# Optimization experiments

Measured on AMD Instinct MI355X. Metric: run time of the kernel, lower is better.

Reference implementation:

```python
import jax, jax.numpy as jnp
import numpy as np


def setup_inputs() -> dict:
    key = jax.random.key(0)
    k0, k1, k2, k3 = jax.random.split(key, 4)
    B, S, D, F, E = 8, 2048, 1024, 2048, 8
    x = jax.random.normal(k0, (B, S, D), dtype=jnp.float32)
    Wg = jax.random.normal(k1, (D, E), dtype=jnp.float32) * 0.02
    W1 = jax.random.normal(k2, (E, D, F), dtype=jnp.float32) * 0.02
    W2 = jax.random.normal(k3, (E, F, D), dtype=jnp.float32) * 0.02
    return {"x": x, "Wg": Wg, "W1": W1, "W2": W2}


def reference(x, Wg, W1, W2):
    # Expert-choice MoE: experts pick top-C tokens, conflicts resolved by
    # max router prob (ties -> lowest expert index, matching the serial loop).
    B, S, D = x.shape
    E = Wg.shape[1]
    T = B * S
    cap = max(1, T // E)  # capacity_factor = 1.0

    xt = x.reshape(T, D)
    logits = xt @ Wg                      # [T, E]
    probs = jax.nn.softmax(logits, axis=-1)
    pT = probs.T                          # [E, T] token affinities per expert

    _, top_idx = jax.lax.top_k(pT, cap)   # [E, cap] tokens chosen by each expert
    sel = jnp.zeros((E, T), dtype=bool).at[jnp.arange(E)[:, None], top_idx].set(True)

    # Serial conflict loop is equivalent to: per token, pick the selecting
    masked = jnp.where(sel, pT, -jnp.inf)
    assigned = sel.any(axis=0)            # [T]
    tok2exp = jnp.where(assigned,
                        jnp.argmax(masked, axis=0),
                        jnp.argmax(pT, axis=0))          # [T] int
    weights = jnp.take_along_axis(probs, tok2exp[:, None], axis=1)[:, 0]  # [T]

    # Dispatch / expert FFN / weighted combine. Loop over the small fixed
    # expert set; masked tokens contribute exactly zero, matching index_add_.
    out = jnp.zeros_like(xt)
    for e in range(E):
        gate = jnp.where(tok2exp == e, weights, 0.0)     # [T]
        h = jax.nn.gelu(xt @ W1[e], approximate=False) @ W2[e]  # [T, D]
        out = out + gate[:, None] * h

    return out.reshape(B, S, D)
```

## Files before the change

kernel.cpp:

```cpp
#include <hip/hip_runtime.h>
#include <hip/hip_bf16.h>
#include <math.h>

#define T_TOK 16384
#define DIM   1024
#define FF    2048
#define NE    8
#define CAPK  2048
#define WL1SZ 4096
#define WL2SZ 2048

typedef unsigned short u16;
typedef unsigned long long u64;
typedef __attribute__((ext_vector_type(8))) short bf16x8;
typedef __attribute__((ext_vector_type(4))) float f32x4;

__device__ __forceinline__ u16 f2bf(float f) {
  __hip_bfloat16 h = __float2bfloat16(f);
  union { __hip_bfloat16 h; u16 u; } c; c.h = h; return c.u;
}

__device__ __forceinline__ float gelu_f(float v) {
  float z = fabsf(v) * 0.70710678118654752f;
  float t = __builtin_amdgcn_rcpf(1.0f + 0.3275911f * z);
  float poly = t * (0.254829592f +
               t * (-0.284496736f +
               t * (1.421413741f +
               t * (-1.453152027f +
               t * 1.061405429f))));
  float ez = __expf(-z * z);
  float erfz = 1.0f - poly * ez;
  erfz = copysignf(erfz, v);
  return 0.5f * v * (1.0f + erfz);
}

__device__ __forceinline__ void async_copy16(const void* g, void* l) {
  __builtin_amdgcn_global_load_lds(
      (const __attribute__((address_space(1))) unsigned int*)g,
      (__attribute__((address_space(3))) unsigned int*)l, 16, 0, 0);
}

__device__ __forceinline__ bf16x8 ds_read16(const char* p) {
  bf16x8 r;
  asm volatile("ds_read_b128 %0, %1"
               : "=&v"(r)
               : "v"((const __attribute__((address_space(3))) char*)p));
  return r;
}

#define LGKM0()                                                                   \
  do {                                                                            \
    asm volatile("s_waitcnt lgkmcnt(0)" ::: "memory");                            \
    __builtin_amdgcn_sched_barrier(0);                                            \
  } while (0)
#define VMW0() asm volatile("s_waitcnt vmcnt(0)" ::: "memory")
#define BAR() asm volatile("s_barrier" ::: "memory")

__global__ __launch_bounds__(256) void prep_k(const float* __restrict__ x,
                                              const float* __restrict__ Wg,
                                              const float* __restrict__ W1,
                                              const float* __restrict__ W2,
                                              float* __restrict__ probs,
                                              float* __restrict__ probsT,
                                              u16* __restrict__ xb,
                                              u16* __restrict__ w1t,
                                              u16* __restrict__ w2t,
                                              u64* __restrict__ key,
                                              int* cnt, int* cnt2, int* gates) {
  __shared__ float tile[64][65];
  int bid = blockIdx.x, tid = threadIdx.x;
  if (bid < 4096) {
    if (tid < 4) key[bid * 4 + tid] = 0ull;
    if (bid == 0 && tid < NE) { cnt[tid] = 0; cnt2[tid] = 0; }
    if (bid == 0 && tid >= 8 && tid < 10) gates[tid - 8] = 0;
    int wid = tid >> 6, lane = tid & 63;
    int t = bid * 4 + wid;
    const float* xr = x + (size_t)t * DIM;
    u16* xbr = xb + (size_t)t * DIM;
    double acc[NE] = {0, 0, 0, 0, 0, 0, 0, 0};
#pragma unroll 1
    for (int it = 0; it < DIM / 64; ++it) {
      int d = it * 64 + lane;
      float xv = xr[d];
      xbr[d] = f2bf(xv);
      const float4* wrow = (const float4*)(Wg + (size_t)d * NE);
      float4 w0 = wrow[0], w1 = wrow[1];
      acc[0] += (double)xv * (double)w0.x;
      acc[1] += (double)xv * (double)w0.y;
      acc[2] += (double)xv * (double)w0.z;
      acc[3] += (double)xv * (double)w0.w;
      acc[4] += (double)xv * (double)w1.x;
      acc[5] += (double)xv * (double)w1.y;
      acc[6] += (double)xv * (double)w1.z;
      acc[7] += (double)xv * (double)w1.w;
    }
#pragma unroll
    for (int e = 0; e < NE; ++e)
      for (int o = 32; o > 0; o >>= 1) acc[e] += __shfl_down(acc[e], o, 64);
    if (lane == 0) {
      float l[NE], mx = -3.0e38f;
#pragma unroll
      for (int e = 0; e < NE; ++e) { l[e] = (float)acc[e]; mx = fmaxf(mx, l[e]); }
      float s = 0.f;
#pragma unroll
      for (int e = 0; e < NE; ++e) { l[e] = expf(l[e] - mx); s += l[e]; }
      float inv = 1.0f / s;
#pragma unroll
      for (int e = 0; e < NE; ++e) {
        float p = l[e] * inv;
        probs[(size_t)t * NE + e] = p;
        probsT[(size_t)e * T_TOK + t] = p;
      }
    }
  } else {
    int tz = bid - 4096;
    int z = tz >> 9, bxy = tz & 511;
    const float* src;
    u16* dst;
    int R, C;
    if (z < 8) { src = W1 + (size_t)z * DIM * FF; dst = w1t + (size_t)z * DIM * FF; R = DIM; C = FF; }
    else       { src = W2 + (size_t)(z - 8) * FF * DIM; dst = w2t + (size_t)(z - 8) * FF * DIM; R = FF; C = DIM; }
    int nbx = C >> 6;
    int bx = bxy % nbx, by = bxy / nbx;
    int r0 = by * 64, c0 = bx * 64;
    int lr = tid >> 4, lc4 = (tid & 15) * 4;
#pragma unroll
    for (int p = 0; p < 4; ++p) {
      float4 v = *(const float4*)(src + (size_t)(r0 + p * 16 + lr) * C + c0 + lc4);
      tile[p * 16 + lr][lc4 + 0] = v.x;
      tile[p * 16 + lr][lc4 + 1] = v.y;
      tile[p * 16 + lr][lc4 + 2] = v.z;
      tile[p * 16 + lr][lc4 + 3] = v.w;
    }
    __syncthreads();
    int oc = tid >> 3, orr = (tid & 7) * 8;
#pragma unroll
    for (int p = 0; p < 2; ++p) {
      int c = p * 32 + oc;
      u16 h[8];
#pragma unroll
      for (int j = 0; j < 8; ++j) h[j] = f2bf(tile[orr + j][c]);
      *(uint4*)(dst + (size_t)(c0 + c) * R + r0 + orr) = *(uint4*)h;
    }
  }
}

__global__ __launch_bounds__(256) void moe_route_k(const float* __restrict__ probsT,
                                                   const float* __restrict__ probs,
                                                   u64* __restrict__ key,
                                                   int* __restrict__ tok2exp,
                                                   float* __restrict__ wgt,
                                                   int* cnt, int* cnt2,
                                                   int* __restrict__ list,
                                                   int* basep, int* wl1, int* wl2,
                                                   int* gates) {
  __shared__ float pcol[T_TOK];
  __shared__ unsigned whist[8][2048];
  __shared__ unsigned hist[2048];
  __shared__ unsigned bcast[2];
  __shared__ unsigned wsum[4];
  __shared__ int wps[4];
  int bid = blockIdx.x, tid = threadIdx.x, wid = tid >> 6, lane = tid & 63;
  if (bid < 8) {
    int e = bid;
    const float4* src4 = (const float4*)(probsT + (size_t)e * T_TOK);
    for (int i = tid; i < T_TOK / 4; i += 256) ((float4*)pcol)[i] = src4[i];
    for (int i = tid; i < 8 * 2048; i += 256) ((unsigned*)whist)[i] = 0;
    unsigned prefix = 0, remaining = CAPK;
#pragma unroll 1
    for (int lvl = 0; lvl < 3; ++lvl) {
      int nb = (lvl == 2) ? 1024 : 2048;
      if (lvl == 0) {
        __syncthreads();
        for (int i = tid; i < T_TOK; i += 256)
          atomicAdd(&whist[wid][__float_as_uint(pcol[i]) >> 21], 1u);
        __syncthreads();
        for (int j = tid; j < 2048; j += 256) {
          unsigned s2 = 0;
#pragma unroll
          for (int w = 0; w < 8; ++w) s2 += whist[w][j];
          hist[j] = s2;
        }
        __syncthreads();
      } else {
        for (int i = tid; i < 2048; i += 256) hist[i] = 0;
        __syncthreads();
        for (int i = tid; i < T_TOK; i += 256) {
          unsigned k = __float_as_uint(pcol[i]);
          bool m = (lvl == 1) ? ((k >> 21) == prefix) : ((k >> 10) == prefix);
          if (m) atomicAdd(&hist[(lvl == 1) ? ((k >> 10) & 2047u) : (k & 1023u)], 1u);
        }
        __syncthreads();
      }
      int nper = nb / 256;
      unsigned cv = 0;
      for (int j = 0; j < nper; ++j) cv += hist[tid * nper + j];
      unsigned s = cv;
#pragma unroll
      for (int o = 1; o < 64; o <<= 1) {
        unsigned tv = __shfl_down(s, o, 64);
        if (lane + o < 64) s += tv;
      }
      if (lane == 0) wsum[wid] = s;
      __syncthreads();
      unsigned above = 0;
      for (int w = wid + 1; w < 4; ++w) above += wsum[w];
      unsigned Sincl = s + above, Sexcl = Sincl - cv;
      if (Sincl >= remaining && Sexcl < remaining) {
        unsigned rem2 = remaining - Sexcl, cum2 = 0;
        for (int j = nper - 1; j >= 0; --j) {
          unsigned h = hist[tid * nper + j];
          if (cum2 + h >= rem2) { bcast[0] = (unsigned)(tid * nper + j); bcast[1] = rem2 - cum2; break; }
          cum2 += h;
        }
      }
      __syncthreads();
      unsigned b = bcast[0];
      remaining = bcast[1];
      prefix = (lvl == 0) ? b : (lvl == 1) ? ((prefix << 11) | b) : ((prefix << 10) | b);
      __syncthreads();
    }
    unsigned vk = prefix;
    int need = (int)remaining;
    const int CH = T_TOK / 256;
    int i0 = tid * CH;
    int myt = 0;
    for (int i = i0; i < i0 + CH; ++i)
      myt += (__float_as_uint(pcol[i]) == vk);
    int p = myt;
#pragma unroll
    for (int o = 1; o < 64; o <<= 1) {
      int tv = __shfl_up(p, o, 64);
      if (lane >= o) p += tv;
    }
    if (lane == 63) wps[wid] = p;
    __syncthreads();
    int wo = 0;
    for (int w = 0; w < wid; ++w) wo += wps[w];
    int run = wo + p - myt;
    u64 ebits = (u64)(7 - e);
    for (int i = i0; i < i0 + CH; ++i) {
      unsigned k = __float_as_uint(pcol[i]);
      bool sv = false;
      if (k > vk) sv = true;
      else if (k == vk) { if (run < need) sv = true; run++; }
      if (sv) atomicMax(&key[i], ((u64)k << 3) | ebits);
    }
    __threadfence();
    __syncthreads();
    if (tid == 0) atomicAdd(&gates[0], 1);
  } else {
    if (tid == 0) {
      while (atomicAdd(&gates[0], 0) < 8) __builtin_amdgcn_s_sleep(8);
    }
    __syncthreads();
    __threadfence();
    int gid = (bid - 8) * 256 + tid;
    u64 k = key[gid];
    int best;
    float bp;
    if (k) {
      best = 7 - (int)(k & 7);
      bp = __uint_as_float((unsigned)(k >> 3));
    } else {
      best = 0; bp = -3.0e38f;
#pragma unroll
      for (int e = 0; e < NE; ++e) {
        float p = probs[(size_t)gid * NE + e];
        if (p > bp) { bp = p; best = e; }
      }
    }
    tok2exp[gid] = best;
    wgt[gid] = bp;
#pragma unroll
    for (int e = 0; e < NE; ++e) {
      u64 m = __ballot(best == e);
      if (best == e && lane == __ffsll(m) - 1) atomicAdd(&cnt[e], (int)__popcll(m));
    }
    __threadfence();
    __syncthreads();
    if (tid == 0) atomicAdd(&gates[1], 1);
    if (tid == 0) {
      while (atomicAdd(&gates[1], 0) < 64) __builtin_amdgcn_s_sleep(8);
    }
    __syncthreads();
    __threadfence();
    int c[NE];
#pragma unroll
    for (int e = 0; e < NE; ++e) c[e] = cnt[e];
    if (gid < NE) {
      int r = 0;
      for (int e = 0; e < gid; ++e) r += c[e];
      basep[gid] = r;
    }
    if (gid < WL1SZ) {
      int e = gid & 7, j = gid >> 3;
      int mte = (c[e] + 127) >> 7;
      wl1[gid] = (j < mte * 16) ? (e | ((j >> 4) << 4) | ((j & 15) << 12)) : -1;
    }
    if (gid >= WL1SZ && gid < WL1SZ + WL2SZ) {
      int g2 = gid - WL1SZ;
      int e = g2 & 7, j = g2 >> 3;
      int mte = (c[e] + 127) >> 7;
      wl2[g2] = (j < mte * 8) ? (e | ((j >> 3) << 4) | ((j & 7) << 12)) : -1;
    }
    int te = tok2exp[gid];
    int bp_e = 0;
#pragma unroll
    for (int e = 0; e < NE; ++e) if (e < te) bp_e += c[e];
    int sl = 0;
#pragma unroll
    for (int e = 0; e < NE; ++e) {
      u64 m = __ballot(te == e);
      if (te == e) {
        int leader = __ffsll(m) - 1;
        int rank = __popcll(m & ((1ull << lane) - 1));
        int b = 0;
        if (lane == leader) b = atomicAdd(&cnt2[e], (int)__popcll(m));
        b = __shfl(b, leader, 64);
        sl = bp_e + b + rank;
      }
    }
    list[sl] = gid;
  }
}


#define MF(M, N_, AV, BV) acc[M][N_] = __builtin_amdgcn_mfma_f32_16x16x32_bf16(BV, AV, acc[M][N_], 0, 0, 0)

#define STG(kt)                                                                   \
  do {                                                                            \
    char* dA = sm;                                                                \
    char* dB = sm + 16384;                                                        \
    size_t ko = (size_t)(kt) * 128;                                               \
    async_copy16(aP0 + ko,      dA + tid * 16);                                   \
    async_copy16(aP1 + ko,      dA + 4096 + tid * 16);                            \
    async_copy16(aP0 + ko + 64, dA + 8192 + tid * 16);                            \
    async_copy16(aP1 + ko + 64, dA + 12288 + tid * 16);                           \
    async_copy16(bP0 + ko,      dB + tid * 16);                                   \
    async_copy16(bP1 + ko,      dB + 4096 + tid * 16);                            \
    async_copy16(bP0 + ko + 64, dB + 8192 + tid * 16);                            \
    async_copy16(bP1 + ko + 64, dB + 12288 + tid * 16);                           \
  } while (0)

#define DSRD(kkoff)                                                               \
  do {                                                                            \
    const char* pa = sm + (kkoff) + wr * 4096 + laneOff;                          \
    const char* pb = sm + 16384 + (kkoff) + wc * 4096 + laneOff;                  \
    a0 = ds_read16(pa);        a1 = ds_read16(pa + 1024);                         \
    a2 = ds_read16(pa + 2048); a3 = ds_read16(pa + 3072);                         \
    b0 = ds_read16(pb);        b1 = ds_read16(pb + 1024);                         \
    b2 = ds_read16(pb + 2048); b3 = ds_read16(pb + 3072);                         \
  } while (0)

#define MFMA16()                                                                  \
  do {                                                                            \
    __builtin_amdgcn_s_setprio(1);                                                \
    MF(0, 0, a0, b0); MF(0, 1, a0, b1); MF(0, 2, a0, b2); MF(0, 3, a0, b3);       \
    MF(1, 0, a1, b0); MF(1, 1, a1, b1); MF(1, 2, a1, b2); MF(1, 3, a1, b3);       \
    MF(2, 0, a2, b0); MF(2, 1, a2, b1); MF(2, 2, a2, b2); MF(2, 3, a2, b3);       \
    MF(3, 0, a3, b0); MF(3, 1, a3, b1); MF(3, 2, a3, b2); MF(3, 3, a3, b3);       \
    __builtin_amdgcn_s_setprio(0);                                                \
  } while (0)

template <int EPI>
__global__ __launch_bounds__(256, 4) void ffn_k(const u16* __restrict__ A,
                                                const u16* __restrict__ Bm,
                                                void* __restrict__ Out,
                                                const int* __restrict__ list,
                                                const float* __restrict__ wgt,
                                                const int* __restrict__ basep,
                                                const int* __restrict__ cnt,
                                                const int* __restrict__ wl) {
  constexpr int K = EPI ? FF : DIM;
  constexpr int N = EPI ? DIM : FF;
  constexpr int KT = K / 64;

  const int wle = wl[blockIdx.x];
  if (wle < 0) return;
  const int e = wle & 15, mt = (wle >> 4) & 255, nt = wle >> 12;
  const int ce = cnt[e];
  const int be = basep[e];

  __shared__ u16 smem[16384];
  __shared__ int toks[128];
  __shared__ float wsc[128];
  char* const sm = (char*)smem;

  const int tid = threadIdx.x;
  if (tid < 128) {
    int r = mt * 128 + tid;
    int tk = (r < ce) ? list[be + r] : list[be];
    toks[tid] = tk;
    if (EPI == 1) wsc[tid] = wgt[tk];
  }
  __syncthreads();

  const int wid = tid >> 6, lane = tid & 63;
  const int wr = wid >> 1, wc = wid & 1;
  (void)wid;
  const int laneOff = ((lane & 15) >> 1) * 128 + (lane & 1) * 64 +
                      (((lane >> 4) << 4) ^ ((((lane & 15) >> 1) & 3) << 4));

  const int r0 = 2 * (tid >> 3) + ((tid & 7) >> 2);
  const int cbl = ((tid & 3) << 4) ^ (((tid >> 3) & 3) << 4);
  const char *aP0, *aP1;
  if (EPI == 0) {
    aP0 = (const char*)(A + (size_t)toks[r0] * K) + cbl;
    aP1 = (const char*)(A + (size_t)toks[r0 + 64] * K) + cbl;
  } else {
    aP0 = (const char*)(A + ((size_t)be + mt * 128 + r0) * K) + cbl;
    aP1 = (const char*)(A + ((size_t)be + mt * 128 + r0 + 64) * K) + cbl;
  }
  const char* bP0 = (const char*)(Bm + ((size_t)e * N + nt * 128 + r0) * K) + cbl;
  const char* bP1 = (const char*)(Bm + ((size_t)e * N + nt * 128 + r0 + 64) * K) + cbl;

  f32x4 acc[4][4];
#pragma unroll
  for (int m = 0; m < 4; ++m)
#pragma unroll
    for (int n = 0; n < 4; ++n) acc[m][n] = (f32x4){0.f, 0.f, 0.f, 0.f};

  bf16x8 a0, a1, a2, a3, b0, b1, b2, b3;

#pragma unroll 1
  for (int kt = 0; kt < KT; ++kt) {
    STG(kt);
    VMW0();
    BAR();
    DSRD(0);
    LGKM0();
    MFMA16();
    DSRD(8192);
    LGKM0();
    MFMA16();
    BAR();
  }

  const int lc = lane & 15, lq = (lane >> 4) * 4;
#pragma unroll
  for (int m = 0; m < 4; ++m) {
    int trow = wr * 64 + m * 16 + lc;
    int grow = mt * 128 + trow;
    if (grow < ce) {
      if (EPI == 0) {
        size_t rowoff = (size_t)(be + grow) * FF + nt * 128 + wc * 64 + lq;
#pragma unroll
        for (int n = 0; n < 4; ++n) {
          ushort4 h4;
          h4.x = f2bf(gelu_f(acc[m][n][0]));
          h4.y = f2bf(gelu_f(acc[m][n][1]));
          h4.z = f2bf(gelu_f(acc[m][n][2]));
          h4.w = f2bf(gelu_f(acc[m][n][3]));
          *(ushort4*)((u16*)Out + rowoff + n * 16) = h4;
        }
      } else {
        float w = wsc[trow];
        size_t rowoff = (size_t)toks[trow] * DIM + nt * 128 + wc * 64 + lq;
#pragma unroll
        for (int n = 0; n < 4; ++n) {
          float4 o = make_float4(w * acc[m][n][0], w * acc[m][n][1],
                                 w * acc[m][n][2], w * acc[m][n][3]);
          *(float4*)((float*)Out + rowoff + n * 16) = o;
        }
      }
    }
  }
}

extern "C" void kernel_launch(void* const* d_in, const int* in_sizes, int n_in,
                              void* d_out, int out_size, void* d_ws, size_t ws_size,
                              hipStream_t stream) {
  (void)in_sizes; (void)n_in; (void)out_size; (void)ws_size;
  const float* x  = (const float*)d_in[0];
  const float* Wg = (const float*)d_in[1];
  const float* W1 = (const float*)d_in[2];
  const float* W2 = (const float*)d_in[3];
  float* out = (float*)d_out;

  char* ws = (char*)d_ws;
  size_t off = 0;
  auto alloc = [&](size_t bytes) -> void* {
    void* p = ws + off;
    off += (bytes + 255) & ~(size_t)255;
    return p;
  };
  u16* xb   = (u16*)alloc((size_t)T_TOK * DIM * 2);
  u16* w1t  = (u16*)alloc((size_t)NE * FF * DIM * 2);
  u16* w2t  = (u16*)alloc((size_t)NE * DIM * FF * 2);
  u16* H    = (u16*)alloc((size_t)(T_TOK + 256) * FF * 2);
  float* probs  = (float*)alloc((size_t)T_TOK * NE * 4);
  float* probsT = (float*)alloc((size_t)NE * T_TOK * 4);
  u64* key      = (u64*)alloc((size_t)T_TOK * 8);
  float* wgt    = (float*)alloc((size_t)T_TOK * 4);
  int* tok2exp  = (int*)alloc((size_t)T_TOK * 4);
  int* list     = (int*)alloc((size_t)T_TOK * 4);
  int* cnt      = (int*)alloc(64);
  int* cnt2     = (int*)alloc(64);
  int* basep    = (int*)alloc(64);
  int* gates    = (int*)alloc(64);
  int* wl1      = (int*)alloc(WL1SZ * 4);
  int* wl2      = (int*)alloc(WL2SZ * 4);

  prep_k<<<4096 + 8192, 256, 0, stream>>>(x, Wg, W1, W2, probs, probsT, xb, w1t, w2t,
                                          key, cnt, cnt2, gates);
  moe_route_k<<<72, 256, 0, stream>>>(probsT, probs, key, tok2exp, wgt, cnt, cnt2,
                                      list, basep, wl1, wl2, gates);
  ffn_k<0><<<WL1SZ, 256, 0, stream>>>(xb, w1t, H, list, wgt, basep, cnt, wl1);
  ffn_k<1><<<WL2SZ, 256, 0, stream>>>(H, w2t, out, list, wgt, basep, cnt, wl2);
}
```

Before: 358.2 us.

## Fuse router, top-k, assignment and weight transpose into one persistent mega-kernel

Merges the prep kernel and the routing kernel into a single launch. Block ranges form stages (router, per-expert top-k, assignment, weight transpose) chained by global-counter spin gates, so the routing stages can overlap with the weight-transpose blocks. The top-k stage now reads probsT directly from global memory instead of staging a 64KB column in LDS, which shrinks shared memory per block. This relies on earlier-indexed blocks being scheduled first, otherwise the spin-waits can deadlock, and it adds a tiny init kernel to reset the gates.

After: 781.4 us. 118% more time.

```diff
diff --git a/kernel.cpp b/kernel.cpp
--- a/kernel.cpp
+++ b/kernel.cpp
@@ -9,6 +9,11 @@
 #define CAPK  2048
 #define WL1SZ 4096
 #define WL2SZ 2048
+
+#define NB_ROUTER 4096
+#define NB_TOPK   8
+#define NB_ASSIGN 64
+#define NB_TRANS  8192
 
 typedef unsigned short u16;
 typedef unsigned long long u64;
@@ -56,7 +61,11 @@
 #define VMW0() asm volatile("s_waitcnt vmcnt(0)" ::: "memory")
 #define BAR() asm volatile("s_barrier" ::: "memory")
 
-__global__ __launch_bounds__(256) void prep_k(const float* __restrict__ x,
+__global__ void init0_k(int* gates) {
+  if (threadIdx.x < 4) gates[threadIdx.x] = 0;
+}
+
+__global__ __launch_bounds__(256) void mega_k(const float* __restrict__ x,
                                               const float* __restrict__ Wg,
                                               const float* __restrict__ W1,
                                               const float* __restrict__ W2,
@@ -66,14 +75,19 @@
                                               u16* __restrict__ w1t,
                                               u16* __restrict__ w2t,
                                               u64* __restrict__ key,
-                                              int* cnt, int* cnt2, int* gates) {
-  __shared__ float tile[64][65];
+                                              int* __restrict__ tok2exp,
+                                              float* __restrict__ wgt,
+                                              int* cnt, int* cnt2,
+                                              int* __restrict__ list,
+                                              int* basep, int* wl1, int* wl2,
+                                              int* gates) {
+  __shared__ char shm[41088];
   int bid = blockIdx.x, tid = threadIdx.x;
-  if (bid < 4096) {
+  int wid = tid >> 6, lane = tid & 63;
+
+  if (bid < NB_ROUTER) {
     if (tid < 4) key[bid * 4 + tid] = 0ull;
     if (bid == 0 && tid < NE) { cnt[tid] = 0; cnt2[tid] = 0; }
-    if (bid == 0 && tid >= 8 && tid < 10) gates[tid - 8] = 0;
-    int wid = tid >> 6, lane = tid & 63;
     int t = bid * 4 + wid;
     const float* xr = x + (size_t)t * DIM;
     u16* xbr = xb + (size_t)t * DIM;
@@ -112,60 +126,24 @@
         probsT[(size_t)e * T_TOK + t] = p;
       }
     }
-  } else {
-    int tz = bid - 4096;
-    int z = tz >> 9, bxy = tz & 511;
-    const float* src;
-    u16* dst;
-    int R, C;
-    if (z < 8) { src = W1 + (size_t)z * DIM * FF; dst = w1t + (size_t)z * DIM * FF; R = DIM; C = FF; }
-    else       { src = W2 + (size_t)(z - 8) * FF * DIM; dst = w2t + (size_t)(z - 8) * FF * DIM; R = FF; C = DIM; }
-    int nbx = C >> 6;
-    int bx = bxy % nbx, by = bxy / nbx;
-    int r0 = by * 64, c0 = bx * 64;
-    int lr = tid >> 4, lc4 = (tid & 15) * 4;
-#pragma unroll
-    for (int p = 0; p < 4; ++p) {
-      float4 v = *(const float4*)(src + (size_t)(r0 + p * 16 + lr) * C + c0 + lc4);
-      tile[p * 16 + lr][lc4 + 0] = v.x;
-      tile[p * 16 + lr][lc4 + 1] = v.y;
-      tile[p * 16 + lr][lc4 + 2] = v.z;
-      tile[p * 16 + lr][lc4 + 3] = v.w;
-    }
-    __syncthreads();
-    int oc = tid >> 3, orr = (tid & 7) * 8;
-#pragma unroll
-    for (int p = 0; p < 2; ++p) {
-      int c = p * 32 + oc;
-      u16 h[8];
-#pragma unroll
-      for (int j = 0; j < 8; ++j) h[j] = f2bf(tile[orr + j][c]);
-      *(uint4*)(dst + (size_t)(c0 + c) * R + r0 + orr) = *(uint4*)h;
-    }
-  }
-}
-
-__global__ __launch_bounds__(256) void moe_route_k(const float* __restrict__ probsT,
-                                                   const float* __restrict__ probs,
-                                                   u64* __restrict__ key,
-                                                   int* __restrict__ tok2exp,
-                                                   float* __restrict__ wgt,
-                                                   int* cnt, int* cnt2,
-                                                   int* __restrict__ list,
-                                                   int* basep, int* wl1, int* wl2,
-                                                   int* gates) {
-  __shared__ float pcol[T_TOK];
-  __shared__ unsigned whist[8][2048];
-  __shared__ unsigned hist[2048];
-  __shared__ unsigned bcast[2];
-  __shared__ unsigned wsum[4];
-  __shared__ int wps[4];
-  int bid = blockIdx.x, tid = threadIdx.x, wid = tid >> 6, lane = tid & 63;
-  if (bid < 8) {
-    int e = bid;
-    const float4* src4 = (const float4*)(probsT + (size_t)e * T_TOK);
-    for (int i = tid; i < T_TOK / 4; i += 256) ((float4*)pcol)[i] = src4[i];
-    for (int i = tid; i < 8 * 2048; i += 256) ((unsigned*)whist)[i] = 0;
+    __threadfence();
+    __syncthreads();
+    if (tid == 0) atomicAdd(&gates[0], 1);
+
+  } else if (bid < NB_ROUTER + NB_TOPK) {
+    unsigned* whist = (unsigned*)shm;
+    unsigned* hist  = (unsigned*)(shm + 32768);
+    unsigned* bcast = (unsigned*)(shm + 40960);
+    unsigned* wsum  = (unsigned*)(shm + 40976);
+    int*      wps   = (int*)(shm + 40992);
+    if (tid == 0) {
+      while (atomicAdd(&gates[0], 0) < NB_ROUTER) __builtin_amdgcn_s_sleep(8);
+    }
+    __syncthreads();
+    __threadfence();
+    int e = bid - NB_ROUTER;
+    const float* pT = probsT + (size_t)e * T_TOK;
+    for (int i = tid; i < 4 * 2048; i += 256) whist[i] = 0;
     unsigned prefix = 0, remaining = CAPK;
 #pragma unroll 1
     for (int lvl = 0; lvl < 3; ++lvl) {
@@ -173,12 +151,12 @@
       if (lvl == 0) {
         __syncthreads();
         for (int i = tid; i < T_TOK; i += 256)
-          atomicAdd(&whist[wid][__float_as_uint(pcol[i]) >> 21], 1u);
+          atomicAdd(&whist[wid * 2048 + (__float_as_uint(pT[i]) >> 21)], 1u);
         __syncthreads();
         for (int j = tid; j < 2048; j += 256) {
           unsigned s2 = 0;
 #pragma unroll
-          for (int w = 0; w < 8; ++w) s2 += whist[w][j];
+          for (int w = 0; w < 4; ++w) s2 += whist[w * 2048 + j];
           hist[j] = s2;
         }
         __syncthreads();
@@ -186,7 +164,7 @@
         for (int i = tid; i < 2048; i += 256) hist[i] = 0;
         __syncthreads();
         for (int i = tid; i < T_TOK; i += 256) {
-          unsigned k = __float_as_uint(pcol[i]);
+          unsigned k = __float_as_uint(pT[i]);
           bool m = (lvl == 1) ? ((k >> 21) == prefix) : ((k >> 10) == prefix);
           if (m) atomicAdd(&hist[(lvl == 1) ? ((k >> 10) & 2047u) : (k & 1023u)], 1u);
         }
@@ -226,7 +204,7 @@
     int i0 = tid * CH;
     int myt = 0;
     for (int i = i0; i < i0 + CH; ++i)
-      myt += (__float_as_uint(pcol[i]) == vk);
+      myt += (__float_as_uint(pT[i]) == vk);
     int p = myt;
 #pragma unroll
     for (int o = 1; o < 64; o <<= 1) {
@@ -240,7 +218,7 @@
     int run = wo + p - myt;
     u64 ebits = (u64)(7 - e);
     for (int i = i0; i < i0 + CH; ++i) {
-      unsigned k = __float_as_uint(pcol[i]);
+      unsigned k = __float_as_uint(pT[i]);
       bool sv = false;
       if (k > vk) sv = true;
       else if (k == vk) { if (run < need) sv = true; run++; }
@@ -248,14 +226,15 @@
     }
     __threadfence();
     __syncthreads();
-    if (tid == 0) atomicAdd(&gates[0], 1);
-  } else {
+    if (tid == 0) atomicAdd(&gates[1], 1);
+
+  } else if (bid < NB_ROUTER + NB_TOPK + NB_ASSIGN) {
     if (tid == 0) {
-      while (atomicAdd(&gates[0], 0) < 8) __builtin_amdgcn_s_sleep(8);
+      while (atomicAdd(&gates[1], 0) < NB_TOPK) __builtin_amdgcn_s_sleep(8);
     }
     __syncthreads();
     __threadfence();
-    int gid = (bid - 8) * 256 + tid;
+    int gid = (bid - NB_ROUTER - NB_TOPK) * 256 + tid;
     u64 k = key[gid];
     int best;
     float bp;
@@ -279,9 +258,9 @@
     }
     __threadfence();
     __syncthreads();
-    if (tid == 0) atomicAdd(&gates[1], 1);
+    if (tid == 0) atomicAdd(&gates[2], 1);
     if (tid == 0) {
-      while (atomicAdd(&gates[1], 0) < 64) __builtin_amdgcn_s_sleep(8);
+      while (atomicAdd(&gates[2], 0) < NB_ASSIGN) __builtin_amdgcn_s_sleep(8);
     }
     __syncthreads();
     __threadfence();
@@ -322,6 +301,38 @@
       }
     }
     list[sl] = gid;
+
+  } else {
+    float (*tile)[65] = (float (*)[65])shm;
+    int tz = bid - (NB_ROUTER + NB_TOPK + NB_ASSIGN);
+    int z = tz >> 9, bxy = tz & 511;
+    const float* src;
+    u16* dst;
+    int R, C;
+    if (z < 8) { src = W1 + (size_t)z * DIM * FF; dst = w1t + (size_t)z * DIM * FF; R = DIM; C = FF; }
+    else       { src = W2 + (size_t)(z - 8) * FF * DIM; dst = w2t + (size_t)(z - 8) * FF * DIM; R = FF; C = DIM; }
+    int nbx = C >> 6;
+    int bx = bxy % nbx, by = bxy / nbx;
+    int r0 = by * 64, c0 = bx * 64;
+    int lr = tid >> 4, lc4 = (tid & 15) * 4;
+#pragma unroll
+    for (int p = 0; p < 4; ++p) {
+      float4 v = *(const float4*)(src + (size_t)(r0 + p * 16 + lr) * C + c0 + lc4);
+      tile[p * 16 + lr][lc4 + 0] = v.x;
+      tile[p * 16 + lr][lc4 + 1] = v.y;
+      tile[p * 16 + lr][lc4 + 2] = v.z;
+      tile[p * 16 + lr][lc4 + 3] = v.w;
+    }
+    __syncthreads();
+    int oc = tid >> 3, orr = (tid & 7) * 8;
+#pragma unroll
+    for (int p = 0; p < 2; ++p) {
+      int c = p * 32 + oc;
+      u16 h[8];
+#pragma unroll
+      for (int j = 0; j < 8; ++j) h[j] = f2bf(tile[orr + j][c]);
+      *(uint4*)(dst + (size_t)(c0 + c) * R + r0 + orr) = *(uint4*)h;
+    }
   }
 }
 
@@ -502,10 +513,10 @@
   int* wl1      = (int*)alloc(WL1SZ * 4);
   int* wl2      = (int*)alloc(WL2SZ * 4);
 
-  prep_k<<<4096 + 8192, 256, 0, stream>>>(x, Wg, W1, W2, probs, probsT, xb, w1t, w2t,
-                                          key, cnt, cnt2, gates);
-  moe_route_k<<<72, 256, 0, stream>>>(probsT, probs, key, tok2exp, wgt, cnt, cnt2,
-                                      list, basep, wl1, wl2, gates);
+  init0_k<<<1, 64, 0, stream>>>(gates);
+  mega_k<<<NB_ROUTER + NB_TOPK + NB_ASSIGN + NB_TRANS, 256, 0, stream>>>(
+      x, Wg, W1, W2, probs, probsT, xb, w1t, w2t, key, tok2exp, wgt,
+      cnt, cnt2, list, basep, wl1, wl2, gates);
   ffn_k<0><<<WL1SZ, 256, 0, stream>>>(xb, w1t, H, list, wgt, basep, cnt, wl1);
   ffn_k<1><<<WL2SZ, 256, 0, stream>>>(H, w2t, out, list, wgt, basep, cnt, wl2);
 }
```
